# Kernel tuning notes

Hardware: AMD Instinct MI355X
Metric: run time of the kernel (lower is better)

## Reference

```python
import jax, jax.numpy as jnp
import numpy as np

B, T, N, F_IN = 8, 16, 1000, 16
E = 16000
H, D = 4, 32          # heads, gat_hidden_shape
HL = 64               # lstm hidden
OUT = 8
NEG_SLOPE = 0.2       # PyG GATConv default


def setup_inputs() -> dict:
    key = jax.random.key(0)
    ks = jax.random.split(key, 10)
    def init(k, shape, fan):
        return (jax.random.normal(k, shape, jnp.float32) / np.sqrt(fan)).astype(jnp.float32)
    x = jax.random.normal(ks[0], (B, T, N, F_IN), jnp.float32)
    edge_index = jax.random.randint(ks[1], (2, E), 0, N)
    W_gat = init(ks[2], (F_IN, H * D), F_IN)       # GATConv lin weight
    att_src = init(ks[3], (H, D), D)
    att_dst = init(ks[4], (H, D), D)
    b_gat = jnp.zeros((H * D,), jnp.float32)
    W_ih = init(ks[5], (4 * HL, H * D), H * D)     # LSTM, gate order i,f,g,o
    W_hh = init(ks[6], (4 * HL, HL), HL)
    b_ih = jnp.zeros((4 * HL,), jnp.float32)
    b_hh = jnp.zeros((4 * HL,), jnp.float32)
    W_clf = init(ks[7], (OUT, HL), HL)
    b_clf = jnp.zeros((OUT,), jnp.float32)
    return {"x": x, "edge_index": edge_index, "W_gat": W_gat, "att_src": att_src,
            "att_dst": att_dst, "b_gat": b_gat, "W_ih": W_ih, "W_hh": W_hh,
            "b_ih": b_ih, "b_hh": b_hh, "W_clf": W_clf, "b_clf": b_clf}


def reference(x, edge_index, W_gat, att_src, att_dst, b_gat,
              W_ih, W_hh, b_ih, b_hh, W_clf, b_clf):
    Bx, Tx, Nx, Fx = x.shape
    x_flat = x.reshape(Bx * Tx, Nx, Fx)
    # PyG GATConv adds self-loops by default
    loop = jnp.arange(Nx)
    src = jnp.concatenate([edge_index[0], loop])
    dst = jnp.concatenate([edge_index[1], loop])

    def gat_graph(xg):  # xg: [N, F]
        xp = (xg @ W_gat).reshape(Nx, H, D)                 # [N,H,D]
        a_s = jnp.einsum('nhd,hd->nh', xp, att_src)         # [N,H]
        a_d = jnp.einsum('nhd,hd->nh', xp, att_dst)
        e = jax.nn.leaky_relu(a_s[src] + a_d[dst], NEG_SLOPE)  # [E+N,H]
        m = jax.ops.segment_max(e, dst, num_segments=Nx)       # per-target softmax
        ex = jnp.exp(e - m[dst])
        denom = jax.ops.segment_sum(ex, dst, num_segments=Nx)
        alpha = ex / denom[dst]                                # [E+N,H]
        out = jax.ops.segment_sum(alpha[..., None] * xp[src], dst, num_segments=Nx)
        return out.reshape(Nx, H * D) + b_gat                  # [N, H*D]

    gat = jax.vmap(gat_graph)(x_flat)          # [B*T, N, H*D]
    gat = jax.nn.relu(gat)
    pooled = gat.max(axis=1)                   # global_max_pool -> [B*T, H*D]
    seq = pooled.reshape(Bx, Tx, H * D)

    h0 = jnp.zeros((Bx, HL), jnp.float32)
    c0 = jnp.zeros((Bx, HL), jnp.float32)

    def step(carry, xt):  # xt: [B, H*D]
        h, c = carry
        gates = xt @ W_ih.T + h @ W_hh.T + b_ih + b_hh
        i, f, g, o = jnp.split(gates, 4, axis=-1)
        i, f, o = jax.nn.sigmoid(i), jax.nn.sigmoid(f), jax.nn.sigmoid(o)
        g = jnp.tanh(g)
        c = f * c + i * g
        h = o * jnp.tanh(c)
        return (h, c), None

    (hT, _), _ = jax.lax.scan(step, (h0, c0), seq.transpose(1, 0, 2))
    return hT @ W_clf.T + b_clf                # [B, OUT]
```

## Files before the change

### kernel.cpp

```cpp
#include <hip/hip_runtime.h>
#include <hip/hip_bf16.h>
#include <stdint.h>

namespace {
constexpr int kB = 8, kT = 16, kN = 1000, kF = 16;
constexpr int kE = 16000;
constexpr int kH = 4, kHD = 128;
constexpr int kHL = 64, kOUT = 8;
constexpr int kG = kB * kT;
constexpr float kNeg = 0.2f;
constexpr int kPre = 1024;
constexpr int kNPW = 32;
constexpr int kBCAP = 64;

constexpr size_t CX_WG   = 0;
constexpr size_t CX_ATS  = CX_WG   + 2048;
constexpr size_t CX_ATD  = CX_ATS  + 128;
constexpr size_t CX_BG   = CX_ATD  + 128;
constexpr size_t CX_WIH  = CX_BG   + 128;
constexpr size_t CX_WHH  = CX_WIH  + 32768;
constexpr size_t CX_BIH  = CX_WHH  + 16384;
constexpr size_t CX_BHH  = CX_BIH  + 256;
constexpr size_t CX_WCLF = CX_BHH  + 256;
constexpr size_t CX_BCLF = CX_WCLF + 512;
constexpr size_t CX_TOTAL = CX_BCLF + 8;

constexpr size_t OFF_FLAG  = 0;
constexpr size_t OFF_ROW   = 256;
constexpr size_t OFF_COL   = 4352;
constexpr size_t OFF_POOL  = 68608;
constexpr size_t OFF_CANON = 134400;
constexpr size_t OFF_AS    = 239872;
constexpr size_t OFF_BUCKET = OFF_AS + (size_t)kG * 288000;
constexpr size_t BUCKET_BYTES = (size_t)kN * kBCAP * 4;
constexpr size_t OFF_PPART  = OFF_BUCKET + 256000;
constexpr size_t PART25_BYTES = (size_t)kG * 25 * kHD * 4;
constexpr size_t PART50_BYTES = (size_t)kG * 50 * kHD * 4;

constexpr int kSetupBlocks = 41;
}

typedef float v2f __attribute__((ext_vector_type(2)));

__device__ __forceinline__ float bf2f(unsigned short u) {
    return __uint_as_float(((uint32_t)u) << 16);
}
__device__ __forceinline__ float blo(uint32_t u) { return __uint_as_float(u << 16); }
__device__ __forceinline__ float bhi(uint32_t u) { return __uint_as_float(u & 0xffff0000u); }
__device__ __forceinline__ unsigned short f2bf(float f) {
    uint32_t u = __float_as_uint(f);
    uint32_t r = (u + 0x7fff + ((u >> 16) & 1)) >> 16;
    return (unsigned short)r;
}
__device__ __forceinline__ float sigm(float x) { return 1.f / (1.f + __expf(-x)); }

__device__ __forceinline__ int detect_isf_wave(const unsigned short* xs, int lane) {
    const uint2 s4 = *(const uint2*)(xs + lane * 4);
    const unsigned short u0 = (unsigned short)(s4.x & 0xffff);
    const unsigned short u1 = (unsigned short)(s4.x >> 16);
    const unsigned short u2 = (unsigned short)(s4.y & 0xffff);
    const unsigned short u3 = (unsigned short)(s4.y >> 16);
    int loc = 0;
#define ISF_TEST(u) { int ex = ((u) >> 7) & 0xff; \
    loc += ((u) == 0 || (ex >= 97 && ex <= 143)) ? 1 : 0; }
    ISF_TEST(u0) ISF_TEST(u1) ISF_TEST(u2) ISF_TEST(u3)
#undef ISF_TEST
#pragma unroll
    for (int sft = 1; sft < 64; sft <<= 1) loc += __shfl_xor(loc, sft, 64);
    return (loc >= 205) ? 0 : 1;
}

struct ConvArgs {
    const unsigned short* src[10];
    int n[10];
};

__global__ __launch_bounds__(256) void mega_setup(
        const void* __restrict__ xraw, const int* __restrict__ ei,
        ConvArgs ca,
        const unsigned short* __restrict__ WgR,
        const unsigned short* __restrict__ atsR,
        const unsigned short* __restrict__ atdR,
        int* __restrict__ flag, int* __restrict__ rowdeg, int* __restrict__ col,
        int* __restrict__ bucket, int use_bucket,
        unsigned short* __restrict__ canon,
        unsigned short* __restrict__ xp_all,
        float* __restrict__ as_all, float* __restrict__ ad_all,
        unsigned int* __restrict__ pooled) {
    const int t = threadIdx.x;
    const unsigned short* xs = (const unsigned short*)xraw;

    if (blockIdx.x < 8) {
        const int isf = detect_isf_wave(xs, t & 63);
        if (blockIdx.x == 0 && t == 0) *flag = isf;
        const int gid = (int)blockIdx.x * 256 + t;
        size_t base = 0;
        for (int s = 0; s < 10; ++s) {
            const int n = ca.n[s];
            if (isf) {
                const float* fp = (const float*)ca.src[s];
                for (int i = gid; i < n; i += 2048) canon[base + i] = f2bf(fp[i]);
            } else {
                const unsigned short* sp = ca.src[s];
                for (int i = gid; i < n; i += 2048) canon[base + i] = sp[i];
            }
            base += (size_t)n;
        }
    } else if (blockIdx.x == 8) {
        for (int i = t; i < kG * kHD; i += 256) pooled[i] = 0u;
    } else if (blockIdx.x < kSetupBlocks) {
        if (use_bucket) {
            const int gid = (int)(blockIdx.x - 9) * 256 + t;
            const int* srcp = ei;
            const int* dstp = ei + kE;
            for (int e = gid; e < kE; e += 32 * 256) {
                const int d = dstp[e];
                const int pos = atomicAdd(&rowdeg[d], 1);
                if (pos < kBCAP) bucket[d * kBCAP + pos] = srcp[e];
            }
        } else if (blockIdx.x == 9) {
            __shared__ int cnt[1024];
            __shared__ int wtot[4];
            const int lane = t & 63, w = t >> 6;
            for (int i = t; i < 1024; i += 256) cnt[i] = 0;
            __syncthreads();
            const int* dst = ei + kE;
            for (int e = t; e < kE; e += 256) atomicAdd(&cnt[dst[e]], 1);
            __syncthreads();
            const int n0 = 4 * t;
            int c0 = cnt[n0], c1 = cnt[n0 + 1], c2 = cnt[n0 + 2], c3 = cnt[n0 + 3];
            int s0 = c0, s1 = s0 + c1, s2 = s1 + c2, s3 = s2 + c3;
            int tot = s3;
#pragma unroll
            for (int sft = 1; sft < 64; sft <<= 1) {
                int v = __shfl_up(tot, sft, 64);
                if (lane >= sft) tot += v;
            }
            if (lane == 63) wtot[w] = tot;
            __syncthreads();
            int wexcl = 0;
            for (int j = 0; j < w; ++j) wexcl += wtot[j];
            const int excl = wexcl + tot - s3;
            if (t == 0) rowdeg[0] = 0;
            if (n0 < kN) {
                rowdeg[n0 + 1] = excl + s0;
                rowdeg[n0 + 2] = excl + s1;
                rowdeg[n0 + 3] = excl + s2;
                rowdeg[n0 + 4] = excl + s3;
            }
            __syncthreads();
            cnt[n0] = excl; cnt[n0 + 1] = excl + s0;
            cnt[n0 + 2] = excl + s1; cnt[n0 + 3] = excl + s2;
            __syncthreads();
            for (int e = t; e < kE; e += 256) {
                int d0 = dst[e];
                int pos = atomicAdd(&cnt[d0], 1);
                col[pos] = ei[e];
            }
        }
    } else {
        const int lane = t & 63;
        const int isf = detect_isf_wave(xs, lane);
        const int wv = t >> 6;
        const int wid = (int)(blockIdx.x - kSetupBlocks) * 4 + wv;

        float wA[kF], wB[kF];
        float as0, as1, ad0, ad1;
        if (isf) {
            const float* wf = (const float*)WgR;
#pragma unroll
            for (int f = 0; f < kF; ++f) {
                const float2 wp = ((const float2*)(wf + (size_t)f * kHD))[lane];
                wA[f] = wp.x; wB[f] = wp.y;
            }
            const float2 sv = ((const float2*)atsR)[lane];
            as0 = sv.x; as1 = sv.y;
            const float2 dv2 = ((const float2*)atdR)[lane];
            ad0 = dv2.x; ad1 = dv2.y;
        } else {
            const uint32_t* w32 = (const uint32_t*)WgR;
#pragma unroll
            for (int f = 0; f < kF; ++f) {
                const uint32_t u = w32[f * 64 + lane];
                wA[f] = blo(u); wB[f] = bhi(u);
            }
            const uint32_t us = ((const uint32_t*)atsR)[lane];
            as0 = blo(us); as1 = bhi(us);
            const uint32_t ud = ((const uint32_t*)atdR)[lane];
            ad0 = blo(ud); ad1 = bhi(ud);
        }

        uint32_t* xp32 = (uint32_t*)xp_all;
        const int nStart = wid * kNPW;
        const int nEnd = min(nStart + kNPW, kG * kN);
        if (nStart >= nEnd) return;

        auto emit = [&](int node, const float* xv) {
            float vA = 0.f, vB = 0.f;
#pragma unroll
            for (int f = 0; f < kF; ++f) {
                vA = fmaf(xv[f], wA[f], vA);
                vB = fmaf(xv[f], wB[f], vB);
            }
            xp32[(size_t)node * 64 + lane] =
                (uint32_t)f2bf(vA) | ((uint32_t)f2bf(vB) << 16);
            float aS = vA * as0 + vB * as1;
            float aD = vA * ad0 + vB * ad1;
#pragma unroll
            for (int sft = 1; sft < 16; sft <<= 1) {
                aS += __shfl_xor(aS, sft, 64);
                aD += __shfl_xor(aD, sft, 64);
            }
            if ((lane & 15) == 0) {
                as_all[(size_t)node * kH + (lane >> 4)] = aS;
                ad_all[(size_t)node * kH + (lane >> 4)] = aD;
            }
        };

        if (isf) {
            const float4* xr = (const float4*)xraw;
            float4 c0 = xr[(size_t)nStart * 4 + 0], c1 = xr[(size_t)nStart * 4 + 1];
            float4 c2 = xr[(size_t)nStart * 4 + 2], c3 = xr[(size_t)nStart * 4 + 3];
            for (int node = nStart; node < nEnd; ++node) {
                const int nn = (node + 1 < nEnd) ? node + 1 : node;
                const float4 p0 = xr[(size_t)nn * 4 + 0];
                const float4 p1 = xr[(size_t)nn * 4 + 1];
                const float4 p2 = xr[(size_t)nn * 4 + 2];
                const float4 p3 = xr[(size_t)nn * 4 + 3];
                const float xv[kF] = {c0.x, c0.y, c0.z, c0.w, c1.x, c1.y, c1.z, c1.w,
                                      c2.x, c2.y, c2.z, c2.w, c3.x, c3.y, c3.z, c3.w};
                emit(node, xv);
                c0 = p0; c1 = p1; c2 = p2; c3 = p3;
            }
        } else {
            const uint4* xr = (const uint4*)xs;
            uint4 c0 = xr[(size_t)nStart * 2 + 0], c1 = xr[(size_t)nStart * 2 + 1];
            for (int node = nStart; node < nEnd; ++node) {
                const int nn = (node + 1 < nEnd) ? node + 1 : node;
                const uint4 p0 = xr[(size_t)nn * 2 + 0];
                const uint4 p1 = xr[(size_t)nn * 2 + 1];
                const float xv[kF] = {
                    blo(c0.x), bhi(c0.x), blo(c0.y), bhi(c0.y),
                    blo(c0.z), bhi(c0.z), blo(c0.w), bhi(c0.w),
                    blo(c1.x), bhi(c1.x), blo(c1.y), bhi(c1.y),
                    blo(c1.z), bhi(c1.z), blo(c1.w), bhi(c1.w)};
                emit(node, xv);
                c0 = p0; c1 = p1;
            }
        }
    }
}

template <int NB>
__global__ __launch_bounds__(256) void gat_aggregate(
        const int* __restrict__ rowdeg, const int* __restrict__ col,
        const int* __restrict__ bucket, int use_bucket,
        const unsigned short* __restrict__ xp,
        const float* __restrict__ a_s, const float* __restrict__ a_d,
        const unsigned short* __restrict__ bg,
        unsigned int* __restrict__ pooled,
        float* __restrict__ part, int use_part) {
    constexpr int NPB = kN / NB;
    constexpr int ITERS = NPB / 4;

    __shared__ float2 colal[4][4][68];
    __shared__ float pm[4][kHD];

    const int w = threadIdx.x >> 6;
    const int lane = threadIdx.x & 63;
    const int sub = lane >> 4;
    const int cl = lane & 15;
    const int hh = cl >> 2;
    const int xcd = blockIdx.x & 7;
    const int j = blockIdx.x >> 3;
    const int gl = xcd + 8 * (j / NB);
    const int blk = j % NB;
    const size_t gn = (size_t)gl * kN;
    const char* xpcl = (const char*)(xp + gn * kHD) + cl * 16;
    const float4* as4 = (const float4*)a_s + gn;
    const float4* ad4 = (const float4*)a_d + gn;
    const uint32_t* bg32 = (const uint32_t*)bg;
    float bgv[8];
#pragma unroll
    for (int jb = 0; jb < 4; ++jb) {
        uint32_t u = bg32[cl * 4 + jb];
        bgv[2 * jb] = blo(u);
        bgv[2 * jb + 1] = bhi(u);
    }
    float pool[8];
#pragma unroll
    for (int jb = 0; jb < 8; ++jb) pool[jb] = 0.f;

    auto pairBody = [&](v2f* acc2, float& dh, int e0) {
        const float2 cA = colal[w][hh][e0 + sub];
        const float2 cB = colal[w][hh][e0 + 4 + sub];
        const uint4 uA = *(const uint4*)(xpcl + __float_as_int(cA.x));
        const uint4 uB = *(const uint4*)(xpcl + __float_as_int(cB.x));
        const float aA = cA.y, aB = cB.y;
        const v2f aA2 = {aA, aA}, aB2 = {aB, aB};
        acc2[0] += aA2 * (v2f){blo(uA.x), bhi(uA.x)};
        acc2[1] += aA2 * (v2f){blo(uA.y), bhi(uA.y)};
        acc2[2] += aA2 * (v2f){blo(uA.z), bhi(uA.z)};
        acc2[3] += aA2 * (v2f){blo(uA.w), bhi(uA.w)};
        acc2[0] += aB2 * (v2f){blo(uB.x), bhi(uB.x)};
        acc2[1] += aB2 * (v2f){blo(uB.y), bhi(uB.y)};
        acc2[2] += aB2 * (v2f){blo(uB.z), bhi(uB.z)};
        acc2[3] += aB2 * (v2f){blo(uB.w), bhi(uB.w)};
        dh += aA + aB;
    };
    auto singleBody = [&](v2f* acc2, float& dh, int e0) {
        const float2 cA = colal[w][hh][e0 + sub];
        const uint4 uA = *(const uint4*)(xpcl + __float_as_int(cA.x));
        const float aA = cA.y;
        const v2f aA2 = {aA, aA};
        acc2[0] += aA2 * (v2f){blo(uA.x), bhi(uA.x)};
        acc2[1] += aA2 * (v2f){blo(uA.y), bhi(uA.y)};
        acc2[2] += aA2 * (v2f){blo(uA.z), bhi(uA.z)};
        acc2[3] += aA2 * (v2f){blo(uA.w), bhi(uA.w)};
        dh += aA;
    };
    auto finishNode = [&](v2f* acc2, float dh) {
        float acc[8];
#pragma unroll
        for (int jb = 0; jb < 4; ++jb) {
            acc[2 * jb] = acc2[jb].x;
            acc[2 * jb + 1] = acc2[jb].y;
        }
#pragma unroll
        for (int jb = 0; jb < 8; ++jb) {
            acc[jb] += __shfl_xor(acc[jb], 16, 64);
            acc[jb] += __shfl_xor(acc[jb], 32, 64);
        }
        dh += __shfl_xor(dh, 16, 64);
        dh += __shfl_xor(dh, 32, 64);
        const float inv = 1.f / dh;
#pragma unroll
        for (int jb = 0; jb < 8; ++jb) {
            const float o = acc[jb] * inv + bgv[jb];
            pool[jb] = fmaxf(pool[jb], o > 0.f ? o : 0.f);
        }
    };

    if (use_bucket) {
        int n0i = blk * NPB + w;
        int degc = min(rowdeg[n0i], 63);
        int sc = (lane < degc) ? bucket[n0i * kBCAP + lane] : n0i;
        float4 avc = as4[sc];
        float4 dvc = ad4[n0i];

        for (int it = 0; it < ITERS; ++it) {
            const int deg = degc;
            const int E = deg + 1;
            const int cntP = (E + 3) & ~3;
            const int s = sc;
            const float4 av = avc;
            const float4 dv = dvc;

            if (lane < cntP) {
                float p0 = 0.f, p1 = 0.f, p2 = 0.f, p3 = 0.f;
                if (lane < E) {
                    float t0 = av.x + dv.x, t1 = av.y + dv.y;
                    float t2 = av.z + dv.z, t3 = av.w + dv.w;
                    t0 = t0 > 0.f ? t0 : kNeg * t0;
                    t1 = t1 > 0.f ? t1 : kNeg * t1;
                    t2 = t2 > 0.f ? t2 : kNeg * t2;
                    t3 = t3 > 0.f ? t3 : kNeg * t3;
                    p0 = __expf(t0); p1 = __expf(t1);
                    p2 = __expf(t2); p3 = __expf(t3);
                }
                const float cf = __int_as_float(s << 8);
                colal[w][0][lane] = make_float2(cf, p0);
                colal[w][1][lane] = make_float2(cf, p1);
                colal[w][2][lane] = make_float2(cf, p2);
                colal[w][3][lane] = make_float2(cf, p3);
            }

            const int itn = (it + 1 == ITERS) ? 0 : (it + 1);
            const int n_nxt = blk * NPB + itn * 4 + w;
            degc = min(rowdeg[n_nxt], 63);
            dvc = ad4[n_nxt];
            sc = (lane < degc) ? bucket[n_nxt * kBCAP + lane] : n_nxt;

            v2f acc2[4];
#pragma unroll
            for (int jb = 0; jb < 4; ++jb) acc2[jb] = (v2f){0.f, 0.f};
            float dh = 0.f;
            int e0 = 0;
            if (cntP >= 8) { pairBody(acc2, dh, 0); e0 = 8; }
            avc = as4[sc];
            for (; e0 + 8 <= cntP; e0 += 8) pairBody(acc2, dh, e0);
            if (e0 < cntP) singleBody(acc2, dh, e0);

            finishNode(acc2, dh);
        }
    } else {
        for (int it = 0; it < ITERS; ++it) {
            const int n = blk * NPB + it * 4 + w;
            const int r0 = rowdeg[n];
            const int deg = rowdeg[n + 1] - r0;
            const int E = deg + 1;
            const float4 dv = ad4[n];
            v2f acc2[4];
#pragma unroll
            for (int jb = 0; jb < 4; ++jb) acc2[jb] = (v2f){0.f, 0.f};
            float dh = 0.f;

            for (int base = 0; base < E; base += 64) {
                const int cnt = min(64, E - base);
                const int cntP = (cnt + 3) & ~3;
                if (lane < cntP) {
                    const int eg = base + lane;
                    const bool act = lane < cnt;
                    const int s = (act && eg < deg) ? col[r0 + eg] : n;
                    float p0 = 0.f, p1 = 0.f, p2 = 0.f, p3 = 0.f;
                    if (act) {
                        const float4 av = as4[s];
                        float t0 = av.x + dv.x, t1 = av.y + dv.y;
                        float t2 = av.z + dv.z, t3 = av.w + dv.w;
                        t0 = t0 > 0.f ? t0 : kNeg * t0;
                        t1 = t1 > 0.f ? t1 : kNeg * t1;
                        t2 = t2 > 0.f ? t2 : kNeg * t2;
                        t3 = t3 > 0.f ? t3 : kNeg * t3;
                        p0 = __expf(t0); p1 = __expf(t1);
                        p2 = __expf(t2); p3 = __expf(t3);
                    }
                    const float cf = __int_as_float(s << 8);
                    colal[w][0][lane] = make_float2(cf, p0);
                    colal[w][1][lane] = make_float2(cf, p1);
                    colal[w][2][lane] = make_float2(cf, p2);
                    colal[w][3][lane] = make_float2(cf, p3);
                }
                int e0 = 0;
                for (; e0 + 8 <= cntP; e0 += 8) pairBody(acc2, dh, e0);
                if (e0 < cntP) singleBody(acc2, dh, e0);
            }
            finishNode(acc2, dh);
        }
    }

    if (sub == 0) {
#pragma unroll
        for (int jb = 0; jb < 8; ++jb) pm[w][cl * 8 + jb] = pool[jb];
    }
    __syncthreads();
    if (w == 0 && sub == 0) {
        if (use_part) {
            float* dst = part + ((size_t)gl * NB + blk) * kHD;
#pragma unroll
            for (int jb = 0; jb < 8; ++jb) {
                const int c = cl * 8 + jb;
                dst[c] = fmaxf(fmaxf(pm[0][c], pm[1][c]), fmaxf(pm[2][c], pm[3][c]));
            }
        } else {
            const size_t gp = (size_t)gl * kHD;
#pragma unroll
            for (int jb = 0; jb < 8; ++jb) {
                const int c = cl * 8 + jb;
                float vmax = fmaxf(fmaxf(pm[0][c], pm[1][c]), fmaxf(pm[2][c], pm[3][c]));
                atomicMax(pooled + gp + c, __float_as_uint(vmax));
            }
        }
    }
}

template <int NB>
__global__ __launch_bounds__(256) void lstm_head(
        const float* __restrict__ pooled, const float* __restrict__ part,
        int use_part,
        const unsigned short* __restrict__ Wih,
        const unsigned short* __restrict__ Whh,
        const unsigned short* __restrict__ bih,
        const unsigned short* __restrict__ bhh,
        const unsigned short* __restrict__ Wclf,
        const unsigned short* __restrict__ bclf,
        const int* __restrict__ flag,
        void* __restrict__ out) {
    const int b = blockIdx.x;
    const int r = threadIdx.x;
    __shared__ float xt[kHD];
    __shared__ float hs[kHL];
    __shared__ float gates[4 * kHL];

    uint32_t wih[64];
    const uint32_t* pw = (const uint32_t*)(Wih + (size_t)r * kHD);
#pragma unroll
    for (int j = 0; j < 64; ++j) wih[j] = pw[j];
    uint32_t whh[32];
    const uint32_t* ph = (const uint32_t*)(Whh + (size_t)r * kHL);
#pragma unroll
    for (int j = 0; j < 32; ++j) whh[j] = ph[j];
    const float bias = bf2f(bih[r]) + bf2f(bhh[r]);

    float c_st = 0.f;
    if (r < kHL) hs[r] = 0.f;
    __syncthreads();

    for (int t = 0; t < kT; ++t) {
        const size_t g = (size_t)b * kT + t;
        if (r < kHD) {
            if (use_part) {
                const float* ps = part + g * (size_t)NB * kHD + r;
                float v = ps[0];
#pragma unroll
                for (int k = 1; k < NB; ++k) v = fmaxf(v, ps[(size_t)k * kHD]);
                xt[r] = v;
            } else {
                xt[r] = pooled[g * kHD + r];
            }
        }
        __syncthreads();
        float a0 = 0.f, a1 = 0.f, a2 = 0.f, a3 = 0.f;
#pragma unroll
        for (int j = 0; j < 64; j += 4) {
            uint32_t u0 = wih[j], u1 = wih[j + 1], u2 = wih[j + 2], u3 = wih[j + 3];
            a0 += blo(u0) * xt[2 * j + 0] + bhi(u0) * xt[2 * j + 1];
            a1 += blo(u1) * xt[2 * j + 2] + bhi(u1) * xt[2 * j + 3];
            a2 += blo(u2) * xt[2 * j + 4] + bhi(u2) * xt[2 * j + 5];
            a3 += blo(u3) * xt[2 * j + 6] + bhi(u3) * xt[2 * j + 7];
        }
#pragma unroll
        for (int j = 0; j < 32; j += 4) {
            uint32_t u0 = whh[j], u1 = whh[j + 1], u2 = whh[j + 2], u3 = whh[j + 3];
            a0 += blo(u0) * hs[2 * j + 0] + bhi(u0) * hs[2 * j + 1];
            a1 += blo(u1) * hs[2 * j + 2] + bhi(u1) * hs[2 * j + 3];
            a2 += blo(u2) * hs[2 * j + 4] + bhi(u2) * hs[2 * j + 5];
            a3 += blo(u3) * hs[2 * j + 6] + bhi(u3) * hs[2 * j + 7];
        }
        gates[r] = bias + (a0 + a1) + (a2 + a3);
        __syncthreads();
        if (r < kHL) {
            const float iv = sigm(gates[r]);
            const float fv = sigm(gates[kHL + r]);
            const float gv = tanhf(gates[2 * kHL + r]);
            const float ov = sigm(gates[3 * kHL + r]);
            c_st = fv * c_st + iv * gv;
            hs[r] = ov * tanhf(c_st);
        }
        __syncthreads();
    }
    if (r < kOUT) {
        float acc = bf2f(bclf[r]);
#pragma unroll
        for (int k = 0; k < kHL; ++k) acc += hs[k] * bf2f(Wclf[r * kHL + k]);
        if (*flag) ((float*)out)[b * kOUT + r] = acc;
        else ((__hip_bfloat16*)out)[b * kOUT + r] = __float2bfloat16(acc);
    }
}

extern "C" void kernel_launch(void* const* d_in, const int* in_sizes, int n_in,
                              void* d_out, int out_size, void* d_ws, size_t ws_size,
                              hipStream_t stream) {
    const int* ei = (const int*)d_in[1];

    char* ws = (char*)d_ws;
    int*            flag   = (int*)(ws + OFF_FLAG);
    int*            rowdeg = (int*)(ws + OFF_ROW);
    int*            colv   = (int*)(ws + OFF_COL);
    unsigned int*   pooled = (unsigned int*)(ws + OFF_POOL);
    unsigned short* canon  = (unsigned short*)(ws + OFF_CANON);

    unsigned short* cBg   = canon + CX_BG;
    unsigned short* cWih  = canon + CX_WIH;
    unsigned short* cWhh  = canon + CX_WHH;
    unsigned short* cBih  = canon + CX_BIH;
    unsigned short* cBhh  = canon + CX_BHH;
    unsigned short* cWclf = canon + CX_WCLF;
    unsigned short* cBclf = canon + CX_BCLF;

    float*          a_s = (float*)(ws + OFF_AS);
    float*          a_d = (float*)(ws + OFF_AS + (size_t)kG * 16000);
    unsigned short* xp  = (unsigned short*)(ws + OFF_AS + (size_t)kG * 32000);

    const int use_bucket = (ws_size >= OFF_PPART) ? 1 : 0;
    const int part50_ok  = (ws_size >= OFF_PPART + PART50_BYTES) ? 1 : 0;
    const int part25_ok  = (ws_size >= OFF_PPART + PART25_BYTES) ? 1 : 0;
    const int use_part   = (part50_ok || part25_ok) ? 1 : 0;
    int* bucket = (int*)(ws + OFF_BUCKET);
    float* part = (float*)(ws + OFF_PPART);

    ConvArgs ca;
    const int sizes[10] = {2048, 128, 128, 128, 32768, 16384, 256, 256, 512, 8};
    const int which[10] = {2, 3, 4, 5, 6, 7, 8, 9, 10, 11};
    for (int i = 0; i < 10; ++i) {
        ca.src[i] = (const unsigned short*)d_in[which[i]];
        ca.n[i] = sizes[i];
    }

    hipMemsetAsync(ws + OFF_ROW, 0, 4096, stream);

    mega_setup<<<kSetupBlocks + kPre, 256, 0, stream>>>(
        d_in[0], ei, ca,
        (const unsigned short*)d_in[2], (const unsigned short*)d_in[3],
        (const unsigned short*)d_in[4],
        flag, rowdeg, colv, bucket, use_bucket, canon, xp, a_s, a_d, pooled);
    if (part50_ok) {
        gat_aggregate<50><<<kG * 50, 256, 0, stream>>>(
            rowdeg, colv, bucket, use_bucket, xp, a_s, a_d, cBg,
            pooled, part, 1);
        lstm_head<50><<<kB, 256, 0, stream>>>((const float*)pooled, part, 1,
                                              cWih, cWhh, cBih, cBhh,
                                              cWclf, cBclf, flag, d_out);
    } else {
        gat_aggregate<25><<<kG * 25, 256, 0, stream>>>(
            rowdeg, colv, bucket, use_bucket, xp, a_s, a_d, cBg,
            pooled, part, use_part);
        lstm_head<25><<<kB, 256, 0, stream>>>((const float*)pooled, part, use_part,
                                              cWih, cWhh, cBih, cBhh,
                                              cWclf, cBclf, flag, d_out);
    }
}
```

Measured before the change: 204.7 us.

## Hoist LSTM input projection out of recurrence into a parallel kernel

Splits the LSTM head into two kernels. The first computes the input-gate projection (W_ih·x_t plus biases) for all 128 timesteps×batches in parallel across 128 blocks, including the partial-max reduction of pooled features. The second runs the sequential recurrence with only the W_hh matvec per step, which shortens the serial critical path that previously ran on just 8 blocks. It adds one extra kernel launch and a small global buffer that reuses the a_s workspace region.

```diff
diff --git a/kernel.cpp b/kernel.cpp
--- a/kernel.cpp
+++ b/kernel.cpp
@@ -464,60 +464,67 @@
 }
 
 template <int NB>
-__global__ __launch_bounds__(256) void lstm_head(
+__global__ __launch_bounds__(256) void lstm_gates_x(
         const float* __restrict__ pooled, const float* __restrict__ part,
         int use_part,
         const unsigned short* __restrict__ Wih,
-        const unsigned short* __restrict__ Whh,
         const unsigned short* __restrict__ bih,
         const unsigned short* __restrict__ bhh,
+        float* __restrict__ gx) {
+    const int g = blockIdx.x;
+    const int r = threadIdx.x;
+    __shared__ float xt[kHD];
+
+    if (r < kHD) {
+        if (use_part) {
+            const float* ps = part + (size_t)g * NB * kHD + r;
+            float v = ps[0];
+#pragma unroll
+            for (int k = 1; k < NB; ++k) v = fmaxf(v, ps[(size_t)k * kHD]);
+            xt[r] = v;
+        } else {
+            xt[r] = pooled[(size_t)g * kHD + r];
+        }
+    }
+    __syncthreads();
+
+    const uint32_t* pw = (const uint32_t*)(Wih + (size_t)r * kHD);
+    float a0 = 0.f, a1 = 0.f, a2 = 0.f, a3 = 0.f;
+#pragma unroll
+    for (int j = 0; j < 64; j += 4) {
+        uint32_t u0 = pw[j], u1 = pw[j + 1], u2 = pw[j + 2], u3 = pw[j + 3];
+        a0 += blo(u0) * xt[2 * j + 0] + bhi(u0) * xt[2 * j + 1];
+        a1 += blo(u1) * xt[2 * j + 2] + bhi(u1) * xt[2 * j + 3];
+        a2 += blo(u2) * xt[2 * j + 4] + bhi(u2) * xt[2 * j + 5];
+        a3 += blo(u3) * xt[2 * j + 6] + bhi(u3) * xt[2 * j + 7];
+    }
+    gx[(size_t)g * 256 + r] = bf2f(bih[r]) + bf2f(bhh[r]) + (a0 + a1) + (a2 + a3);
+}
+
+__global__ __launch_bounds__(256) void lstm_seq(
+        const float* __restrict__ gx,
+        const unsigned short* __restrict__ Whh,
         const unsigned short* __restrict__ Wclf,
         const unsigned short* __restrict__ bclf,
         const int* __restrict__ flag,
         void* __restrict__ out) {
     const int b = blockIdx.x;
     const int r = threadIdx.x;
-    __shared__ float xt[kHD];
     __shared__ float hs[kHL];
     __shared__ float gates[4 * kHL];
 
-    uint32_t wih[64];
-    const uint32_t* pw = (const uint32_t*)(Wih + (size_t)r * kHD);
-#pragma unroll
-    for (int j = 0; j < 64; ++j) wih[j] = pw[j];
     uint32_t whh[32];
     const uint32_t* ph = (const uint32_t*)(Whh + (size_t)r * kHL);
 #pragma unroll
     for (int j = 0; j < 32; ++j) whh[j] = ph[j];
-    const float bias = bf2f(bih[r]) + bf2f(bhh[r]);
 
     float c_st = 0.f;
     if (r < kHL) hs[r] = 0.f;
     __syncthreads();
 
     for (int t = 0; t < kT; ++t) {
-        const size_t g = (size_t)b * kT + t;
-        if (r < kHD) {
-            if (use_part) {
-                const float* ps = part + g * (size_t)NB * kHD + r;
-                float v = ps[0];
-#pragma unroll
-                for (int k = 1; k < NB; ++k) v = fmaxf(v, ps[(size_t)k * kHD]);
-                xt[r] = v;
-            } else {
-                xt[r] = pooled[g * kHD + r];
-            }
-        }
-        __syncthreads();
+        const float gxv = gx[((size_t)b * kT + t) * 256 + r];
         float a0 = 0.f, a1 = 0.f, a2 = 0.f, a3 = 0.f;
-#pragma unroll
-        for (int j = 0; j < 64; j += 4) {
-            uint32_t u0 = wih[j], u1 = wih[j + 1], u2 = wih[j + 2], u3 = wih[j + 3];
-            a0 += blo(u0) * xt[2 * j + 0] + bhi(u0) * xt[2 * j + 1];
-            a1 += blo(u1) * xt[2 * j + 2] + bhi(u1) * xt[2 * j + 3];
-            a2 += blo(u2) * xt[2 * j + 4] + bhi(u2) * xt[2 * j + 5];
-            a3 += blo(u3) * xt[2 * j + 6] + bhi(u3) * xt[2 * j + 7];
-        }
 #pragma unroll
         for (int j = 0; j < 32; j += 4) {
             uint32_t u0 = whh[j], u1 = whh[j + 1], u2 = whh[j + 2], u3 = whh[j + 3];
@@ -526,7 +533,7 @@
             a2 += blo(u2) * hs[2 * j + 4] + bhi(u2) * hs[2 * j + 5];
             a3 += blo(u3) * hs[2 * j + 6] + bhi(u3) * hs[2 * j + 7];
         }
-        gates[r] = bias + (a0 + a1) + (a2 + a3);
+        gates[r] = gxv + (a0 + a1) + (a2 + a3);
         __syncthreads();
         if (r < kHL) {
             const float iv = sigm(gates[r]);
@@ -570,6 +577,7 @@
     float*          a_s = (float*)(ws + OFF_AS);
     float*          a_d = (float*)(ws + OFF_AS + (size_t)kG * 16000);
     unsigned short* xp  = (unsigned short*)(ws + OFF_AS + (size_t)kG * 32000);
+    float*          gx  = (float*)(ws + OFF_AS);
 
     const int use_bucket = (ws_size >= OFF_PPART) ? 1 : 0;
     const int part50_ok  = (ws_size >= OFF_PPART + PART50_BYTES) ? 1 : 0;
@@ -597,15 +605,14 @@
         gat_aggregate<50><<<kG * 50, 256, 0, stream>>>(
             rowdeg, colv, bucket, use_bucket, xp, a_s, a_d, cBg,
             pooled, part, 1);
-        lstm_head<50><<<kB, 256, 0, stream>>>((const float*)pooled, part, 1,
-                                              cWih, cWhh, cBih, cBhh,
-                                              cWclf, cBclf, flag, d_out);
+        lstm_gates_x<50><<<kG, 256, 0, stream>>>(
+            (const float*)pooled, part, 1, cWih, cBih, cBhh, gx);
     } else {
         gat_aggregate<25><<<kG * 25, 256, 0, stream>>>(
             rowdeg, colv, bucket, use_bucket, xp, a_s, a_d, cBg,
             pooled, part, use_part);
-        lstm_head<25><<<kB, 256, 0, stream>>>((const float*)pooled, part, use_part,
-                                              cWih, cWhh, cBih, cBhh,
-                                              cWclf, cBclf, flag, d_out);
-    }
-}
+        lstm_gates_x<25><<<kG, 256, 0, stream>>>(
+            (const float*)pooled, part, use_part, cWih, cBih, cBhh, gx);
+    }
+    lstm_seq<<<kB, 256, 0, stream>>>(gx, cWhh, cWclf, cBclf, flag, d_out);
+}
```

Measured after the change: 185.9 us. -9.2%, faster.
